# Optimization experiments

Hardware: AMD Instinct MI355X
Metric: run time of the kernel (lower is better)

## Reference

```python
import jax, jax.numpy as jnp
import numpy as np
import math

B = 256
IMG_H = IMG_W = 256
GH = GW = 64
HID = 512
NUM_GLIMPSES = 8


def _filterbank(delta_caps, center_caps, image_size, glimpse_size):
    # delta_caps, center_caps: (B,) in [-1, 1]
    I = float(image_size)
    G = float(glimpse_size)
    centers = (I - 1.0) * (center_caps + 1.0) / 2.0            # (B,)
    deltas = I / G * (1.0 - jnp.abs(delta_caps))               # (B,)
    gammas = jnp.exp(1.0 - 2.0 * jnp.abs(delta_caps))          # (B,)
    glimpse_pixels = jnp.arange(glimpse_size, dtype=jnp.float32) - (G - 1.0) / 2.0  # (G,)
    gp = centers[:, None] + deltas[:, None] * glimpse_pixels[None, :]               # (B, G)
    image_pixels = jnp.arange(image_size, dtype=jnp.float32)                        # (I,)
    fx = (image_pixels[None, None, :] - gp[:, :, None]) / gammas[:, None, None]     # (B, G, I)
    fx = 1.0 / (math.pi * gammas[:, None, None] * (1.0 + fx * fx))
    fx = fx / (jnp.sum(fx, axis=2, keepdims=True) + 1e-4)
    return jnp.transpose(fx, (0, 2, 1))  # (B, I, G)


def setup_inputs() -> dict:
    key = jax.random.key(0)
    ks = jax.random.split(key, 7)
    in_dim = GH * GW  # channels=1 (images come in as (B, h, w))
    return {
        "image_pairs": jax.random.normal(ks[0], (B, 2, IMG_H, IMG_W), dtype=jnp.float32),
        "W_ih": jax.random.normal(ks[1], (4 * HID, in_dim), dtype=jnp.float32) * 0.02,
        "W_hh": jax.random.normal(ks[2], (4 * HID, HID), dtype=jnp.float32) * 0.02,
        "b_ih": jax.random.normal(ks[3], (4 * HID,), dtype=jnp.float32) * 0.02,
        "b_hh": jax.random.normal(ks[4], (4 * HID,), dtype=jnp.float32) * 0.02,
        "W_g": jax.random.normal(ks[5], (3, HID), dtype=jnp.float32) * 0.02,
        "b_g": jax.random.normal(ks[6], (3,), dtype=jnp.float32) * 0.02,
    }


def _arc_forward(image_pairs, W_ih, W_hh, b_ih, b_hh, W_g, b_g):
    batch = image_pairs.shape[0]
    img0 = image_pairs[:, 0].astype(jnp.float32)  # (B, H, W)
    img1 = image_pairs[:, 1].astype(jnp.float32)

    def step(carry, t):
        Hx, Cx = carry
        images = jnp.where(t == 0, img0, img1)  # turn parity selects image
        gp = jnp.tanh(Hx @ W_g.T + b_g)         # (B, 3): (h_center, w_center, delta)
        F_h = _filterbank(gp[:, 2], gp[:, 0], IMG_H, GH)  # (B, H, GH)
        F_w = _filterbank(gp[:, 2], gp[:, 1], IMG_W, GW)  # (B, W, GW)
        # F_h^T @ images @ F_w  -> (B, GH, GW)
        g = jnp.einsum('bhg,bhw->bgw', F_h, images)
        g = jnp.einsum('bgw,bwj->bgj', g, F_w)
        x = g.reshape(batch, -1)  # (B, GH*GW)
        gates = x @ W_ih.T + b_ih + Hx @ W_hh.T + b_hh  # (B, 4*HID)
        i, f, gg, o = jnp.split(gates, 4, axis=1)       # torch LSTMCell gate order
        Cx = jax.nn.sigmoid(f) * Cx + jax.nn.sigmoid(i) * jnp.tanh(gg)
        Hx = jax.nn.sigmoid(o) * jnp.tanh(Cx)
        return (Hx, Cx), Hx

    init = (jnp.zeros((batch, HID), jnp.float32), jnp.zeros((batch, HID), jnp.float32))
    turns = jnp.arange(2 * NUM_GLIMPSES) % 2
    (Hx, Cx), all_hidden = jax.lax.scan(step, init, turns)
    return all_hidden[-1]  # (B, HID), last hidden state


def reference(image_pairs, W_ih, W_hh, b_ih, b_hh, W_g, b_g):
    return _arc_forward(image_pairs, W_ih, W_hh, b_ih, b_hh, W_g, b_g)
```

## Files before the change

kernel.cpp:

```cpp
#include <hip/hip_runtime.h>
#include <math.h>

#define NB 256
#define IMG 256
#define GSZ 64
#define HID 512
#define NSTEP 16
#define KTOT 4608
#define SPLITK 8
#define KCHUNK 576
#define KSTEPS 18

#define GP 264
#define SP 40
#define GLDS_BYTES (4*64*GP*2 + 512)

typedef unsigned short u16;
typedef __attribute__((ext_vector_type(8))) short s16x8;
typedef __attribute__((ext_vector_type(4))) float f32x4;

__device__ inline u16 f2bf(float f) {
    unsigned u = __float_as_uint(f);
    unsigned r = u + 0x7fffu + ((u >> 16) & 1u);
    return (u16)(r >> 16);
}
__device__ inline float bf2f(u16 h) { return __uint_as_float((unsigned)h << 16); }

__global__ __launch_bounds__(256) void k_wsplit(const float* __restrict__ W_ih,
                                                const float* __restrict__ W_hh,
                                                u16* __restrict__ wc_hi,
                                                u16* __restrict__ wc_lo) {
    const int nchunk = 2048 * KTOT / 4;
    const int stride = gridDim.x * blockDim.x;
    for (int c = blockIdx.x * blockDim.x + threadIdx.x; c < nchunk; c += stride) {
        const int j = c / (KTOT / 4);
        const int k = (c - j * (KTOT / 4)) * 4;
        float4 v;
        if (k < 4096) v = *(const float4*)&W_ih[(size_t)j * 4096 + k];
        else          v = *(const float4*)&W_hh[(size_t)j * 512 + (k - 4096)];
        float f[4] = {v.x, v.y, v.z, v.w};
        u16 hi[4], lo[4];
        #pragma unroll
        for (int i = 0; i < 4; ++i) {
            hi[i] = f2bf(f[i]);
            lo[i] = f2bf(f[i] - bf2f(hi[i]));
        }
        const size_t o = (size_t)j * KTOT + k;
        *(ushort4*)&wc_hi[o] = make_ushort4(hi[0], hi[1], hi[2], hi[3]);
        *(ushort4*)&wc_lo[o] = make_ushort4(lo[0], lo[1], lo[2], lo[3]);
    }
}

__global__ __launch_bounds__(64) void k_params(const float* __restrict__ Hx,
                                               const float* __restrict__ W_g,
                                               const float* __restrict__ b_g,
                                               float* __restrict__ params) {
    const int b = blockIdx.x;
    const int l = threadIdx.x;
    float s0 = 0.f, s1 = 0.f, s2 = 0.f;
    const float* h = Hx + (size_t)b * HID;
    for (int k = l; k < HID; k += 64) {
        float hv = h[k];
        s0 += hv * W_g[k];
        s1 += hv * W_g[HID + k];
        s2 += hv * W_g[2 * HID + k];
    }
    for (int off = 32; off; off >>= 1) {
        s0 += __shfl_xor(s0, off, 64);
        s1 += __shfl_xor(s1, off, 64);
        s2 += __shfl_xor(s2, off, 64);
    }
    if (l == 0) {
        float g0 = tanhf(s0 + b_g[0]);
        float g1 = tanhf(s1 + b_g[1]);
        float g2 = tanhf(s2 + b_g[2]);
        float ad = fabsf(g2);
        params[b * 4 + 0] = 127.5f * (g0 + 1.0f);
        params[b * 4 + 1] = 127.5f * (g1 + 1.0f);
        params[b * 4 + 2] = 4.0f * (1.0f - ad);
        params[b * 4 + 3] = expf(1.0f - 2.0f * ad);
    }
}

__global__ __launch_bounds__(256, 1) void k_glimpse(const float* __restrict__ params,
                                                    const float* __restrict__ imgs,
                                                    int sel,
                                                    u16* __restrict__ xh,
                                                    u16* __restrict__ xl) {
    extern __shared__ u16 sm[];
    u16* FwH  = sm;
    u16* FwL  = sm + 64 * GP;
    u16* R2   = sm + 2 * 64 * GP;
    u16* AstH = R2;
    u16* AstL = R2 + 256 * SP;
    u16* FhH  = R2;
    u16* FhL  = R2 + 64 * GP;
    float* invW = (float*)(sm + 4 * 64 * GP);
    float* invA = invW + 64;

    const int b = blockIdx.x, t = threadIdx.x;
    const int lane = t & 63, wv = t >> 6;
    const int fr = lane & 15, kg = lane >> 4;
    const float ch = params[b * 4 + 0];
    const float cw = params[b * 4 + 1];
    const float dl = params[b * 4 + 2];
    const float gm = params[b * 4 + 3];
    const float ig = 1.0f / gm;
    const float coef = 1.0f / (3.14159265358979323846f * gm);

    {
        const int r  = t >> 2;
        const int w0 = (t & 3) * 64;
        const float rc = cw + dl * ((float)r - 31.5f);
        float s = 0.f;
        for (int i = 0; i < 64; i += 4) {
            u16 hh[4], ll[4];
            #pragma unroll
            for (int j = 0; j < 4; ++j) {
                float u = ((float)(w0 + i + j) - rc) * ig;
                float val = coef / (1.0f + u * u);
                s += val;
                hh[j] = f2bf(val);
                ll[j] = f2bf(val - bf2f(hh[j]));
            }
            *(ushort4*)&FwH[r * GP + w0 + i] = make_ushort4(hh[0], hh[1], hh[2], hh[3]);
            *(ushort4*)&FwL[r * GP + w0 + i] = make_ushort4(ll[0], ll[1], ll[2], ll[3]);
        }
        s += __shfl_xor(s, 1, 64);
        s += __shfl_xor(s, 2, 64);
        if ((t & 3) == 0) invW[r] = 1.0f / (s + 1e-4f);
    }
    __syncthreads();

    const float* imgp = imgs + (size_t)(b * 2 + sel) * (IMG * IMG);
    int rowA[8], coA[8];
    float4 pf[8];
    #pragma unroll
    for (int q = 0; q < 8; ++q) {
        const int c = q * 256 + t;
        rowA[q] = c >> 3;
        coA[q]  = (c & 7) * 4;
        pf[q] = *(const float4*)&imgp[rowA[q] * IMG + coA[q]];
    }
    f32x4 acc[4][4];
    #pragma unroll
    for (int mi = 0; mi < 4; ++mi)
        #pragma unroll
        for (int ni = 0; ni < 4; ++ni) acc[mi][ni] = (f32x4)(0.f);

    for (int ks = 0; ks < 8; ++ks) {
        __syncthreads();
        #pragma unroll
        for (int q = 0; q < 8; ++q) {
            float f[4] = {pf[q].x, pf[q].y, pf[q].z, pf[q].w};
            u16 hh[4], ll[4];
            #pragma unroll
            for (int j = 0; j < 4; ++j) {
                hh[j] = f2bf(f[j]);
                ll[j] = f2bf(f[j] - bf2f(hh[j]));
            }
            *(ushort4*)&AstH[rowA[q] * SP + coA[q]] = make_ushort4(hh[0], hh[1], hh[2], hh[3]);
            *(ushort4*)&AstL[rowA[q] * SP + coA[q]] = make_ushort4(ll[0], ll[1], ll[2], ll[3]);
        }
        __syncthreads();
        if (ks < 7) {
            #pragma unroll
            for (int q = 0; q < 8; ++q)
                pf[q] = *(const float4*)&imgp[rowA[q] * IMG + (ks + 1) * 32 + coA[q]];
        }
        s16x8 ah[4], al[4], bh[4], bl[4];
        #pragma unroll
        for (int mi = 0; mi < 4; ++mi) {
            const int r = wv * 64 + mi * 16 + fr;
            ah[mi] = *(const s16x8*)&AstH[r * SP + kg * 8];
            al[mi] = *(const s16x8*)&AstL[r * SP + kg * 8];
        }
        #pragma unroll
        for (int ni = 0; ni < 4; ++ni) {
            const int r = ni * 16 + fr;
            bh[ni] = *(const s16x8*)&FwH[r * GP + ks * 32 + kg * 8];
            bl[ni] = *(const s16x8*)&FwL[r * GP + ks * 32 + kg * 8];
        }
        #pragma unroll
        for (int mi = 0; mi < 4; ++mi)
            #pragma unroll
            for (int ni = 0; ni < 4; ++ni) {
                acc[mi][ni] = __builtin_amdgcn_mfma_f32_16x16x32_bf16(ah[mi], bh[ni], acc[mi][ni], 0, 0, 0);
                acc[mi][ni] = __builtin_amdgcn_mfma_f32_16x16x32_bf16(ah[mi], bl[ni], acc[mi][ni], 0, 0, 0);
                acc[mi][ni] = __builtin_amdgcn_mfma_f32_16x16x32_bf16(al[mi], bh[ni], acc[mi][ni], 0, 0, 0);
            }
    }
    __syncthreads();

    #pragma unroll
    for (int ni = 0; ni < 4; ++ni) {
        const int col = ni * 16 + fr;
        const float s = invW[col];
        #pragma unroll
        for (int mi = 0; mi < 4; ++mi) {
            const int hbase = wv * 64 + mi * 16 + kg * 4;
            u16 hh[4], ll[4];
            #pragma unroll
            for (int r = 0; r < 4; ++r) {
                float v = acc[mi][ni][r] * s;
                hh[r] = f2bf(v);
                ll[r] = f2bf(v - bf2f(hh[r]));
            }
            *(ushort4*)&FwH[col * GP + hbase] = make_ushort4(hh[0], hh[1], hh[2], hh[3]);
            *(ushort4*)&FwL[col * GP + hbase] = make_ushort4(ll[0], ll[1], ll[2], ll[3]);
        }
    }

    {
        const int r  = t >> 2;
        const int h0 = (t & 3) * 64;
        const float rc = ch + dl * ((float)r - 31.5f);
        float s = 0.f;
        for (int i = 0; i < 64; i += 4) {
            u16 hh[4], ll[4];
            #pragma unroll
            for (int j = 0; j < 4; ++j) {
                float u = ((float)(h0 + i + j) - rc) * ig;
                float val = coef / (1.0f + u * u);
                s += val;
                hh[j] = f2bf(val);
                ll[j] = f2bf(val - bf2f(hh[j]));
            }
            *(ushort4*)&FhH[r * GP + h0 + i] = make_ushort4(hh[0], hh[1], hh[2], hh[3]);
            *(ushort4*)&FhL[r * GP + h0 + i] = make_ushort4(ll[0], ll[1], ll[2], ll[3]);
        }
        s += __shfl_xor(s, 1, 64);
        s += __shfl_xor(s, 2, 64);
        if ((t & 3) == 0) invA[r] = 1.0f / (s + 1e-4f);
    }
    __syncthreads();

    f32x4 acc2[4];
    #pragma unroll
    for (int ni = 0; ni < 4; ++ni) acc2[ni] = (f32x4)(0.f);

    #pragma unroll
    for (int ks = 0; ks < 8; ++ks) {
        const int ra = wv * 16 + fr;
        s16x8 a2h = *(const s16x8*)&FhH[ra * GP + ks * 32 + kg * 8];
        s16x8 a2l = *(const s16x8*)&FhL[ra * GP + ks * 32 + kg * 8];
        #pragma unroll
        for (int ni = 0; ni < 4; ++ni) {
            const int rb = ni * 16 + fr;
            s16x8 b2h = *(const s16x8*)&FwH[rb * GP + ks * 32 + kg * 8];
            s16x8 b2l = *(const s16x8*)&FwL[rb * GP + ks * 32 + kg * 8];
            acc2[ni] = __builtin_amdgcn_mfma_f32_16x16x32_bf16(a2h, b2h, acc2[ni], 0, 0, 0);
            acc2[ni] = __builtin_amdgcn_mfma_f32_16x16x32_bf16(a2h, b2l, acc2[ni], 0, 0, 0);
            acc2[ni] = __builtin_amdgcn_mfma_f32_16x16x32_bf16(a2l, b2h, acc2[ni], 0, 0, 0);
        }
    }
    const int rbase = wv * 16 + kg * 4;
    float ia[4];
    #pragma unroll
    for (int r = 0; r < 4; ++r) ia[r] = invA[rbase + r];
    u16* xho = xh + (size_t)b * KTOT;
    u16* xlo = xl + (size_t)b * KTOT;
    #pragma unroll
    for (int ni = 0; ni < 4; ++ni) {
        const int col = ni * 16 + fr;
        #pragma unroll
        for (int r = 0; r < 4; ++r) {
            float v = acc2[ni][r] * ia[r];
            u16 hv = f2bf(v);
            const int o = (rbase + r) * GSZ + col;
            xho[o] = hv;
            xlo[o] = f2bf(v - bf2f(hv));
        }
    }
}

__global__ __launch_bounds__(256) void k_gates(const u16* __restrict__ xcat_hi,
                                               const u16* __restrict__ xcat_lo,
                                               const u16* __restrict__ wc_hi,
                                               const u16* __restrict__ wc_lo,
                                               float* __restrict__ part) {
    __shared__ u16 smem[4][128][40];

    const int bid = blockIdx.x;
    const int mb = bid & 1;
    const int nb = (bid >> 1) & 15;
    const int kc = bid >> 5;
    const int m0 = mb * 128, n0 = nb * 128, k0 = kc * KCHUNK;
    const int t = threadIdx.x;
    const int lane = t & 63, wid = t >> 6;
    const int wm = wid >> 1, wn = wid & 1;
    const int fr = lane & 15, kg = lane >> 4;

    const u16* srcs[8];
    u16* dsts[8];
    #pragma unroll
    for (int q = 0; q < 8; ++q) {
        const int idx = ((q * 256 + t) & 511);
        const int row = idx >> 2;
        const int ko = (idx & 3) * 8;
        const int mat = q >> 1;
        const u16* gbase;
        if (mat == 0)      gbase = xcat_hi + (size_t)(m0 + row) * KTOT;
        else if (mat == 1) gbase = xcat_lo + (size_t)(m0 + row) * KTOT;
        else if (mat == 2) gbase = wc_hi + (size_t)(n0 + row) * KTOT;
        else               gbase = wc_lo + (size_t)(n0 + row) * KTOT;
        srcs[q] = gbase + k0 + ko;
        dsts[q] = &smem[mat][row][ko];
    }

    f32x4 acc[4][4];
    #pragma unroll
    for (int mi = 0; mi < 4; ++mi)
        #pragma unroll
        for (int ni = 0; ni < 4; ++ni) acc[mi][ni] = (f32x4)(0.f);

    s16x8 ld[8];
    #pragma unroll
    for (int q = 0; q < 8; ++q) ld[q] = *(const s16x8*)(srcs[q]);

    for (int ks = 0; ks < KSTEPS; ++ks) {
        __syncthreads();
        #pragma unroll
        for (int q = 0; q < 8; ++q) {
            *(s16x8*)(dsts[q]) = ld[q];
            srcs[q] += 32;
        }
        __syncthreads();
        if (ks + 1 < KSTEPS) {
            #pragma unroll
            for (int q = 0; q < 8; ++q) ld[q] = *(const s16x8*)(srcs[q]);
        }
        s16x8 ah[4], al[4], bh[4], bl[4];
        #pragma unroll
        for (int mi = 0; mi < 4; ++mi) {
            const int r = wm * 64 + mi * 16 + fr;
            ah[mi] = *(const s16x8*)&smem[0][r][kg * 8];
            al[mi] = *(const s16x8*)&smem[1][r][kg * 8];
        }
        #pragma unroll
        for (int ni = 0; ni < 4; ++ni) {
            const int r = wn * 64 + ni * 16 + fr;
            bh[ni] = *(const s16x8*)&smem[2][r][kg * 8];
            bl[ni] = *(const s16x8*)&smem[3][r][kg * 8];
        }
        #pragma unroll
        for (int mi = 0; mi < 4; ++mi)
            #pragma unroll
            for (int ni = 0; ni < 4; ++ni) {
                acc[mi][ni] = __builtin_amdgcn_mfma_f32_16x16x32_bf16(ah[mi], bh[ni], acc[mi][ni], 0, 0, 0);
                acc[mi][ni] = __builtin_amdgcn_mfma_f32_16x16x32_bf16(ah[mi], bl[ni], acc[mi][ni], 0, 0, 0);
                acc[mi][ni] = __builtin_amdgcn_mfma_f32_16x16x32_bf16(al[mi], bh[ni], acc[mi][ni], 0, 0, 0);
            }
    }

    float* pp = part + ((size_t)kc << 19);
    #pragma unroll
    for (int mi = 0; mi < 4; ++mi) {
        const int mbase = m0 + wm * 64 + mi * 16 + (lane >> 4) * 4;
        #pragma unroll
        for (int ni = 0; ni < 4; ++ni) {
            const int col = n0 + wn * 64 + ni * 16 + (lane & 15);
            #pragma unroll
            for (int r = 0; r < 4; ++r)
                pp[(size_t)(mbase + r) * 2048 + col] = acc[mi][ni][r];
        }
    }
}

__global__ __launch_bounds__(256) void k_lstm(const float* __restrict__ part,
                                              const float* __restrict__ b_ih,
                                              const float* __restrict__ b_hh,
                                              float* __restrict__ Cx,
                                              float* __restrict__ Hx,
                                              float* __restrict__ out,
                                              u16* __restrict__ xcat_hi,
                                              u16* __restrict__ xcat_lo) {
    const int id = blockIdx.x * 256 + threadIdx.x;
    const int b = id >> 9, u = id & (HID - 1);
    float gi = b_ih[u] + b_hh[u];
    float gf = b_ih[HID + u] + b_hh[HID + u];
    float gg = b_ih[2 * HID + u] + b_hh[2 * HID + u];
    float go = b_ih[3 * HID + u] + b_hh[3 * HID + u];
    const float* pb = part + (size_t)b * 2048;
    #pragma unroll
    for (int kc = 0; kc < SPLITK; ++kc) {
        const float* p = pb + (size_t)kc * (256 * 2048);
        gi += p[u];
        gf += p[HID + u];
        gg += p[2 * HID + u];
        go += p[3 * HID + u];
    }
    float si = 1.0f / (1.0f + expf(-gi));
    float sf = 1.0f / (1.0f + expf(-gf));
    float so = 1.0f / (1.0f + expf(-go));
    float c = sf * Cx[id] + si * tanhf(gg);
    float h = so * tanhf(c);
    Cx[id] = c;
    Hx[id] = h;
    out[id] = h;
    u16 hh = f2bf(h);
    xcat_hi[(size_t)b * KTOT + 4096 + u] = hh;
    xcat_lo[(size_t)b * KTOT + 4096 + u] = f2bf(h - bf2f(hh));
}

extern "C" void kernel_launch(void* const* d_in, const int* in_sizes, int n_in,
                              void* d_out, int out_size, void* d_ws, size_t ws_size,
                              hipStream_t stream) {
    const float* imgs = (const float*)d_in[0];
    const float* W_ih = (const float*)d_in[1];
    const float* W_hh = (const float*)d_in[2];
    const float* b_ih = (const float*)d_in[3];
    const float* b_hh = (const float*)d_in[4];
    const float* W_g  = (const float*)d_in[5];
    const float* b_g  = (const float*)d_in[6];
    float* out = (float*)d_out;

    char* w = (char*)d_ws;
    float* params  = (float*)w;  w += 4096;
    float* Hx      = (float*)w;  w += NB * HID * 4;
    float* Cx      = (float*)w;  w += NB * HID * 4;
    u16* xcat_hi   = (u16*)w;    w += (size_t)NB * KTOT * 2;
    u16* xcat_lo   = (u16*)w;    w += (size_t)NB * KTOT * 2;
    u16* wc_hi     = (u16*)w;    w += (size_t)2048 * KTOT * 2;
    u16* wc_lo     = (u16*)w;    w += (size_t)2048 * KTOT * 2;
    float* part    = (float*)w;  w += (size_t)SPLITK * NB * 2048 * 4;

    (void)hipFuncSetAttribute((const void*)k_glimpse,
                              hipFuncAttributeMaxDynamicSharedMemorySize, GLDS_BYTES);

    hipMemsetAsync(Hx, 0, (size_t)2 * NB * HID * sizeof(float), stream);
    hipMemsetAsync(xcat_hi, 0, (size_t)2 * NB * KTOT * 2, stream);

    k_wsplit<<<2304, 256, 0, stream>>>(W_ih, W_hh, wc_hi, wc_lo);

    for (int step = 0; step < NSTEP; ++step) {
        k_params<<<NB, 64, 0, stream>>>(Hx, W_g, b_g, params);
        k_glimpse<<<NB, 256, GLDS_BYTES, stream>>>(params, imgs, step & 1, xcat_hi, xcat_lo);
        k_gates<<<256, 256, 0, stream>>>(xcat_hi, xcat_lo, wc_hi, wc_lo, part);
        k_lstm<<<NB * HID / 256, 256, 0, stream>>>(part, b_ih, b_hh, Cx, Hx, out, xcat_hi, xcat_lo);
    }
}
```

Before: 1.020 ms.

## Fuse all LSTM glimpse steps into one persistent kernel with grid barriers

New measurement: 3.205 ms. 214% more time.

```diff
diff --git a/kernel.cpp b/kernel.cpp
--- a/kernel.cpp
+++ b/kernel.cpp
@@ -10,10 +10,8 @@
 #define SPLITK 8
 #define KCHUNK 576
 #define KSTEPS 18
-
-#define GP 264
 #define SP 40
-#define GLDS_BYTES (4*64*GP*2 + 512)
+#define TP 72
 
 typedef unsigned short u16;
 typedef __attribute__((ext_vector_type(8))) short s16x8;
@@ -25,382 +23,421 @@
     return (u16)(r >> 16);
 }
 __device__ inline float bf2f(u16 h) { return __uint_as_float((unsigned)h << 16); }
-
-__global__ __launch_bounds__(256) void k_wsplit(const float* __restrict__ W_ih,
-                                                const float* __restrict__ W_hh,
-                                                u16* __restrict__ wc_hi,
-                                                u16* __restrict__ wc_lo) {
-    const int nchunk = 2048 * KTOT / 4;
-    const int stride = gridDim.x * blockDim.x;
-    for (int c = blockIdx.x * blockDim.x + threadIdx.x; c < nchunk; c += stride) {
-        const int j = c / (KTOT / 4);
-        const int k = (c - j * (KTOT / 4)) * 4;
-        float4 v;
-        if (k < 4096) v = *(const float4*)&W_ih[(size_t)j * 4096 + k];
-        else          v = *(const float4*)&W_hh[(size_t)j * 512 + (k - 4096)];
-        float f[4] = {v.x, v.y, v.z, v.w};
-        u16 hi[4], lo[4];
-        #pragma unroll
-        for (int i = 0; i < 4; ++i) {
-            hi[i] = f2bf(f[i]);
-            lo[i] = f2bf(f[i] - bf2f(hi[i]));
-        }
-        const size_t o = (size_t)j * KTOT + k;
-        *(ushort4*)&wc_hi[o] = make_ushort4(hi[0], hi[1], hi[2], hi[3]);
-        *(ushort4*)&wc_lo[o] = make_ushort4(lo[0], lo[1], lo[2], lo[3]);
+__device__ inline float sigm(float v) { return 1.0f / (1.0f + expf(-v)); }
+
+__device__ inline void gridbar(int* bar, int gen) {
+    __threadfence();
+    __syncthreads();
+    const int b = blockIdx.x, t = threadIdx.x;
+    if (b == 0) {
+        if (t > 0) {
+            while (__hip_atomic_load(&bar[1 + t], __ATOMIC_ACQUIRE,
+                                     __HIP_MEMORY_SCOPE_AGENT) < gen)
+                __builtin_amdgcn_s_sleep(2);
+        }
+        __syncthreads();
+        if (t == 0)
+            __hip_atomic_store(&bar[0], gen, __ATOMIC_RELEASE,
+                               __HIP_MEMORY_SCOPE_AGENT);
+    } else {
+        if (t == 0) {
+            __hip_atomic_store(&bar[1 + b], gen, __ATOMIC_RELEASE,
+                               __HIP_MEMORY_SCOPE_AGENT);
+            while (__hip_atomic_load(&bar[0], __ATOMIC_ACQUIRE,
+                                     __HIP_MEMORY_SCOPE_AGENT) < gen)
+                __builtin_amdgcn_s_sleep(2);
+        }
+        __syncthreads();
     }
 }
 
-__global__ __launch_bounds__(64) void k_params(const float* __restrict__ Hx,
-                                               const float* __restrict__ W_g,
-                                               const float* __restrict__ b_g,
-                                               float* __restrict__ params) {
-    const int b = blockIdx.x;
-    const int l = threadIdx.x;
-    float s0 = 0.f, s1 = 0.f, s2 = 0.f;
-    const float* h = Hx + (size_t)b * HID;
-    for (int k = l; k < HID; k += 64) {
-        float hv = h[k];
-        s0 += hv * W_g[k];
-        s1 += hv * W_g[HID + k];
-        s2 += hv * W_g[2 * HID + k];
-    }
-    for (int off = 32; off; off >>= 1) {
-        s0 += __shfl_xor(s0, off, 64);
-        s1 += __shfl_xor(s1, off, 64);
-        s2 += __shfl_xor(s2, off, 64);
-    }
-    if (l == 0) {
-        float g0 = tanhf(s0 + b_g[0]);
-        float g1 = tanhf(s1 + b_g[1]);
-        float g2 = tanhf(s2 + b_g[2]);
-        float ad = fabsf(g2);
-        params[b * 4 + 0] = 127.5f * (g0 + 1.0f);
-        params[b * 4 + 1] = 127.5f * (g1 + 1.0f);
-        params[b * 4 + 2] = 4.0f * (1.0f - ad);
-        params[b * 4 + 3] = expf(1.0f - 2.0f * ad);
-    }
-}
-
-__global__ __launch_bounds__(256, 1) void k_glimpse(const float* __restrict__ params,
-                                                    const float* __restrict__ imgs,
-                                                    int sel,
-                                                    u16* __restrict__ xh,
-                                                    u16* __restrict__ xl) {
-    extern __shared__ u16 sm[];
-    u16* FwH  = sm;
-    u16* FwL  = sm + 64 * GP;
-    u16* R2   = sm + 2 * 64 * GP;
-    u16* AstH = R2;
-    u16* AstL = R2 + 256 * SP;
-    u16* FhH  = R2;
-    u16* FhL  = R2 + 64 * GP;
-    float* invW = (float*)(sm + 4 * 64 * GP);
-    float* invA = invW + 64;
+__global__ __launch_bounds__(256, 2) void k_all(
+    const float* __restrict__ imgs, const float* __restrict__ W_ih,
+    const float* __restrict__ W_hh, const float* __restrict__ b_ih,
+    const float* __restrict__ b_hh, const float* __restrict__ W_g,
+    const float* __restrict__ b_g,
+    int* __restrict__ bar,
+    u16* __restrict__ wc_hi, u16* __restrict__ wc_lo,
+    u16* __restrict__ xcat_hi, u16* __restrict__ xcat_lo,
+    float* __restrict__ part, float* __restrict__ out)
+{
+    __shared__ __align__(16) u16 sm[25600];
+    __shared__ float invW[64];
+    __shared__ float invA[64];
+    __shared__ float red[12];
+    u16* AstH = sm;
+    u16* AstL = sm + 10240;
+    u16* FwcH = sm + 20480;
+    u16* FwcL = sm + 23040;
+    u16* t1TH = sm;
+    u16* t1TL = sm + 4608;
+    u16* FhcH = sm + 9216;
+    u16* FhcL = sm + 13824;
+    u16 (*gsm)[128][40] = (u16 (*)[128][40])sm;
 
     const int b = blockIdx.x, t = threadIdx.x;
     const int lane = t & 63, wv = t >> 6;
     const int fr = lane & 15, kg = lane >> 4;
-    const float ch = params[b * 4 + 0];
-    const float cw = params[b * 4 + 1];
-    const float dl = params[b * 4 + 2];
-    const float gm = params[b * 4 + 3];
-    const float ig = 1.0f / gm;
-    const float coef = 1.0f / (3.14159265358979323846f * gm);
+
+    float hx0 = 0.f, hx1 = 0.f, cx0 = 0.f, cx1 = 0.f;
 
     {
-        const int r  = t >> 2;
-        const int w0 = (t & 3) * 64;
-        const float rc = cw + dl * ((float)r - 31.5f);
-        float s = 0.f;
-        for (int i = 0; i < 64; i += 4) {
-            u16 hh[4], ll[4];
-            #pragma unroll
-            for (int j = 0; j < 4; ++j) {
-                float u = ((float)(w0 + i + j) - rc) * ig;
-                float val = coef / (1.0f + u * u);
-                s += val;
-                hh[j] = f2bf(val);
-                ll[j] = f2bf(val - bf2f(hh[j]));
-            }
-            *(ushort4*)&FwH[r * GP + w0 + i] = make_ushort4(hh[0], hh[1], hh[2], hh[3]);
-            *(ushort4*)&FwL[r * GP + w0 + i] = make_ushort4(ll[0], ll[1], ll[2], ll[3]);
-        }
-        s += __shfl_xor(s, 1, 64);
-        s += __shfl_xor(s, 2, 64);
-        if ((t & 3) == 0) invW[r] = 1.0f / (s + 1e-4f);
+        const int nchunk = 2048 * KTOT / 4;
+        for (int c = b * 256 + t; c < nchunk; c += 65536) {
+            const int j = c / (KTOT / 4);
+            const int k = (c - j * (KTOT / 4)) * 4;
+            float4 v;
+            if (k < 4096) v = *(const float4*)&W_ih[(size_t)j * 4096 + k];
+            else          v = *(const float4*)&W_hh[(size_t)j * 512 + (k - 4096)];
+            float f[4] = {v.x, v.y, v.z, v.w};
+            u16 hi[4], lo[4];
+            #pragma unroll
+            for (int i = 0; i < 4; ++i) {
+                hi[i] = f2bf(f[i]);
+                lo[i] = f2bf(f[i] - bf2f(hi[i]));
+            }
+            const size_t o = (size_t)j * KTOT + k;
+            *(ushort4*)&wc_hi[o] = make_ushort4(hi[0], hi[1], hi[2], hi[3]);
+            *(ushort4*)&wc_lo[o] = make_ushort4(lo[0], lo[1], lo[2], lo[3]);
+        }
     }
-    __syncthreads();
-
-    const float* imgp = imgs + (size_t)(b * 2 + sel) * (IMG * IMG);
-    int rowA[8], coA[8];
-    float4 pf[8];
-    #pragma unroll
-    for (int q = 0; q < 8; ++q) {
-        const int c = q * 256 + t;
-        rowA[q] = c >> 3;
-        coA[q]  = (c & 7) * 4;
-        pf[q] = *(const float4*)&imgp[rowA[q] * IMG + coA[q]];
-    }
-    f32x4 acc[4][4];
-    #pragma unroll
-    for (int mi = 0; mi < 4; ++mi)
-        #pragma unroll
-        for (int ni = 0; ni < 4; ++ni) acc[mi][ni] = (f32x4)(0.f);
-
-    for (int ks = 0; ks < 8; ++ks) {
-        __syncthreads();
+
+    for (int step = 0; step < NSTEP; ++step) {
+        if (step == 0) {
+            const size_t o = (size_t)b * KTOT + 4096 + t;
+            xcat_hi[o] = 0;       xcat_lo[o] = 0;
+            xcat_hi[o + 256] = 0; xcat_lo[o + 256] = 0;
+        } else {
+            #pragma unroll
+            for (int half = 0; half < 2; ++half) {
+                const int u = t + half * 256;
+                float gi = b_ih[u] + b_hh[u];
+                float gf = b_ih[HID + u] + b_hh[HID + u];
+                float gg = b_ih[2 * HID + u] + b_hh[2 * HID + u];
+                float go = b_ih[3 * HID + u] + b_hh[3 * HID + u];
+                const float* pb = part + (size_t)b * 2048;
+                #pragma unroll
+                for (int kc = 0; kc < SPLITK; ++kc) {
+                    const float* p = pb + (size_t)kc * (256 * 2048);
+                    gi += p[u];
+                    gf += p[HID + u];
+                    gg += p[2 * HID + u];
+                    go += p[3 * HID + u];
+                }
+                float co = half ? cx1 : cx0;
+                float c = sigm(gf) * co + sigm(gi) * tanhf(gg);
+                float h = sigm(go) * tanhf(c);
+                if (half) { cx1 = c; hx1 = h; } else { cx0 = c; hx0 = h; }
+                u16 hh = f2bf(h);
+                xcat_hi[(size_t)b * KTOT + 4096 + u] = hh;
+                xcat_lo[(size_t)b * KTOT + 4096 + u] = f2bf(h - bf2f(hh));
+            }
+        }
+        float s0 = hx0 * W_g[t] + hx1 * W_g[t + 256];
+        float s1 = hx0 * W_g[HID + t] + hx1 * W_g[HID + t + 256];
+        float s2 = hx0 * W_g[2 * HID + t] + hx1 * W_g[2 * HID + t + 256];
+        for (int off = 32; off; off >>= 1) {
+            s0 += __shfl_xor(s0, off, 64);
+            s1 += __shfl_xor(s1, off, 64);
+            s2 += __shfl_xor(s2, off, 64);
+        }
+        __syncthreads();
+        if (lane == 0) { red[wv * 3 + 0] = s0; red[wv * 3 + 1] = s1; red[wv * 3 + 2] = s2; }
+        __syncthreads();
+        s0 = red[0] + red[3] + red[6] + red[9];
+        s1 = red[1] + red[4] + red[7] + red[10];
+        s2 = red[2] + red[5] + red[8] + red[11];
+        const float g0 = tanhf(s0 + b_g[0]);
+        const float g1 = tanhf(s1 + b_g[1]);
+        const float g2 = tanhf(s2 + b_g[2]);
+        const float ad = fabsf(g2);
+        const float ch = 127.5f * (g0 + 1.0f);
+        const float cw = 127.5f * (g1 + 1.0f);
+        const float dl = 4.0f * (1.0f - ad);
+        const float gm = expf(1.0f - 2.0f * ad);
+        const float ig = 1.0f / gm;
+        const float coef = 1.0f / (3.14159265358979323846f * gm);
+
+        const int fwr = t >> 2;
+        const int fwc = (t & 3) * 8;
+        const float rcw = cw + dl * ((float)fwr - 31.5f);
+        float rsW = 0.f;
+
+        const float* imgp = imgs + (size_t)(b * 2 + (step & 1)) * (IMG * IMG);
+        int rowA[8], coA[8];
+        float4 pf[8];
         #pragma unroll
         for (int q = 0; q < 8; ++q) {
-            float f[4] = {pf[q].x, pf[q].y, pf[q].z, pf[q].w};
-            u16 hh[4], ll[4];
-            #pragma unroll
-            for (int j = 0; j < 4; ++j) {
-                hh[j] = f2bf(f[j]);
-                ll[j] = f2bf(f[j] - bf2f(hh[j]));
-            }
-            *(ushort4*)&AstH[rowA[q] * SP + coA[q]] = make_ushort4(hh[0], hh[1], hh[2], hh[3]);
-            *(ushort4*)&AstL[rowA[q] * SP + coA[q]] = make_ushort4(ll[0], ll[1], ll[2], ll[3]);
-        }
-        __syncthreads();
-        if (ks < 7) {
-            #pragma unroll
-            for (int q = 0; q < 8; ++q)
-                pf[q] = *(const float4*)&imgp[rowA[q] * IMG + (ks + 1) * 32 + coA[q]];
-        }
-        s16x8 ah[4], al[4], bh[4], bl[4];
+            const int c = q * 256 + t;
+            rowA[q] = c >> 3;
+            coA[q]  = (c & 7) * 4;
+            pf[q] = *(const float4*)&imgp[rowA[q] * IMG + coA[q]];
+        }
+        f32x4 acc[4][4];
+        #pragma unroll
+        for (int mi = 0; mi < 4; ++mi)
+            #pragma unroll
+            for (int ni = 0; ni < 4; ++ni) acc[mi][ni] = (f32x4)(0.f);
+
+        for (int ks = 0; ks < 8; ++ks) {
+            __syncthreads();
+            #pragma unroll
+            for (int q = 0; q < 8; ++q) {
+                float f[4] = {pf[q].x, pf[q].y, pf[q].z, pf[q].w};
+                u16 hh[4], ll[4];
+                #pragma unroll
+                for (int j = 0; j < 4; ++j) {
+                    hh[j] = f2bf(f[j]);
+                    ll[j] = f2bf(f[j] - bf2f(hh[j]));
+                }
+                *(ushort4*)&AstH[rowA[q] * SP + coA[q]] = make_ushort4(hh[0], hh[1], hh[2], hh[3]);
+                *(ushort4*)&AstL[rowA[q] * SP + coA[q]] = make_ushort4(ll[0], ll[1], ll[2], ll[3]);
+            }
+            {
+                u16 hh[8], ll[8];
+                #pragma unroll
+                for (int j = 0; j < 8; ++j) {
+                    float u = ((float)(ks * 32 + fwc + j) - rcw) * ig;
+                    float val = coef / (1.0f + u * u);
+                    rsW += val;
+                    hh[j] = f2bf(val);
+                    ll[j] = f2bf(val - bf2f(hh[j]));
+                }
+                *(ushort4*)&FwcH[fwr * SP + fwc]     = make_ushort4(hh[0], hh[1], hh[2], hh[3]);
+                *(ushort4*)&FwcH[fwr * SP + fwc + 4] = make_ushort4(hh[4], hh[5], hh[6], hh[7]);
+                *(ushort4*)&FwcL[fwr * SP + fwc]     = make_ushort4(ll[0], ll[1], ll[2], ll[3]);
+                *(ushort4*)&FwcL[fwr * SP + fwc + 4] = make_ushort4(ll[4], ll[5], ll[6], ll[7]);
+            }
+            __syncthreads();
+            if (ks < 7) {
+                #pragma unroll
+                for (int q = 0; q < 8; ++q)
+                    pf[q] = *(const float4*)&imgp[rowA[q] * IMG + (ks + 1) * 32 + coA[q]];
+            }
+            s16x8 ah[4], al[4], bh[4], bl[4];
+            #pragma unroll
+            for (int mi = 0; mi < 4; ++mi) {
+                const int r = mi * 16 + fr;
+                ah[mi] = *(const s16x8*)&FwcH[r * SP + kg * 8];
+                al[mi] = *(const s16x8*)&FwcL[r * SP + kg * 8];
+            }
+            #pragma unroll
+            for (int ni = 0; ni < 4; ++ni) {
+                const int r = wv * 64 + ni * 16 + fr;
+                bh[ni] = *(const s16x8*)&AstH[r * SP + kg * 8];
+                bl[ni] = *(const s16x8*)&AstL[r * SP + kg * 8];
+            }
+            #pragma unroll
+            for (int mi = 0; mi < 4; ++mi)
+                #pragma unroll
+                for (int ni = 0; ni < 4; ++ni) {
+                    acc[mi][ni] = __builtin_amdgcn_mfma_f32_16x16x32_bf16(ah[mi], bh[ni], acc[mi][ni], 0, 0, 0);
+                    acc[mi][ni] = __builtin_amdgcn_mfma_f32_16x16x32_bf16(ah[mi], bl[ni], acc[mi][ni], 0, 0, 0);
+                    acc[mi][ni] = __builtin_amdgcn_mfma_f32_16x16x32_bf16(al[mi], bh[ni], acc[mi][ni], 0, 0, 0);
+                }
+        }
+        rsW += __shfl_xor(rsW, 1, 64);
+        rsW += __shfl_xor(rsW, 2, 64);
+        if ((t & 3) == 0) invW[fwr] = 1.0f / (rsW + 1e-4f);
+        __syncthreads();
         #pragma unroll
         for (int mi = 0; mi < 4; ++mi) {
-            const int r = wv * 64 + mi * 16 + fr;
-            ah[mi] = *(const s16x8*)&AstH[r * SP + kg * 8];
-            al[mi] = *(const s16x8*)&AstL[r * SP + kg * 8];
-        }
+            float w4[4];
+            #pragma unroll
+            for (int r = 0; r < 4; ++r) w4[r] = invW[mi * 16 + kg * 4 + r];
+            #pragma unroll
+            for (int ni = 0; ni < 4; ++ni)
+                #pragma unroll
+                for (int r = 0; r < 4; ++r) acc[mi][ni][r] *= w4[r];
+        }
+
+        f32x4 xacc[4];
         #pragma unroll
-        for (int ni = 0; ni < 4; ++ni) {
-            const int r = ni * 16 + fr;
-            bh[ni] = *(const s16x8*)&FwH[r * GP + ks * 32 + kg * 8];
-            bl[ni] = *(const s16x8*)&FwL[r * GP + ks * 32 + kg * 8];
-        }
+        for (int ni = 0; ni < 4; ++ni) xacc[ni] = (f32x4)(0.f);
+        const int fhr = t >> 2;
+        const int fhc = (t & 3) * 16;
+        const float rch = ch + dl * ((float)fhr - 31.5f);
+        float rsA = 0.f;
+
+        for (int p = 0; p < 4; ++p) {
+            __syncthreads();
+            #pragma unroll
+            for (int blk = 0; blk < 4; ++blk) {
+                u16 hh[4], ll[4];
+                #pragma unroll
+                for (int j = 0; j < 4; ++j) {
+                    float u = ((float)(p * 64 + fhc + blk * 4 + j) - rch) * ig;
+                    float val = coef / (1.0f + u * u);
+                    rsA += val;
+                    hh[j] = f2bf(val);
+                    ll[j] = f2bf(val - bf2f(hh[j]));
+                }
+                *(ushort4*)&FhcH[fhr * TP + fhc + blk * 4] = make_ushort4(hh[0], hh[1], hh[2], hh[3]);
+                *(ushort4*)&FhcL[fhr * TP + fhc + blk * 4] = make_ushort4(ll[0], ll[1], ll[2], ll[3]);
+            }
+            if (wv == p) {
+                #pragma unroll
+                for (int mi = 0; mi < 4; ++mi)
+                    #pragma unroll
+                    for (int ni = 0; ni < 4; ++ni)
+                        #pragma unroll
+                        for (int r = 0; r < 4; ++r) {
+                            const int row = mi * 16 + kg * 4 + r;
+                            const int col = ni * 16 + fr;
+                            float v = acc[mi][ni][r];
+                            u16 hv = f2bf(v);
+                            t1TH[row * TP + col] = hv;
+                            t1TL[row * TP + col] = f2bf(v - bf2f(hv));
+                        }
+            }
+            __syncthreads();
+            #pragma unroll
+            for (int k2 = 0; k2 < 2; ++k2) {
+                const int ra = wv * 16 + fr;
+                s16x8 a2h = *(const s16x8*)&FhcH[ra * TP + k2 * 32 + kg * 8];
+                s16x8 a2l = *(const s16x8*)&FhcL[ra * TP + k2 * 32 + kg * 8];
+                #pragma unroll
+                for (int ni = 0; ni < 4; ++ni) {
+                    const int rb = ni * 16 + fr;
+                    s16x8 b2h = *(const s16x8*)&t1TH[rb * TP + k2 * 32 + kg * 8];
+                    s16x8 b2l = *(const s16x8*)&t1TL[rb * TP + k2 * 32 + kg * 8];
+                    xacc[ni] = __builtin_amdgcn_mfma_f32_16x16x32_bf16(a2h, b2h, xacc[ni], 0, 0, 0);
+                    xacc[ni] = __builtin_amdgcn_mfma_f32_16x16x32_bf16(a2h, b2l, xacc[ni], 0, 0, 0);
+                    xacc[ni] = __builtin_amdgcn_mfma_f32_16x16x32_bf16(a2l, b2h, xacc[ni], 0, 0, 0);
+                }
+            }
+        }
+        rsA += __shfl_xor(rsA, 1, 64);
+        rsA += __shfl_xor(rsA, 2, 64);
+        if ((t & 3) == 0) invA[fhr] = 1.0f / (rsA + 1e-4f);
+        __syncthreads();
+        {
+            float ia[4];
+            #pragma unroll
+            for (int r = 0; r < 4; ++r) ia[r] = invA[wv * 16 + kg * 4 + r];
+            u16* xho = xcat_hi + (size_t)b * KTOT;
+            u16* xlo = xcat_lo + (size_t)b * KTOT;
+            #pragma unroll
+            for (int ni = 0; ni < 4; ++ni) {
+                const int col = ni * 16 + fr;
+                #pragma unroll
+                for (int r = 0; r < 4; ++r) {
+                    float v = xacc[ni][r] * ia[r];
+                    u16 hv = f2bf(v);
+                    const int o = (wv * 16 + kg * 4 + r) * GSZ + col;
+                    xho[o] = hv;
+                    xlo[o] = f2bf(v - bf2f(hv));
+                }
+            }
+        }
+        gridbar(bar, 2 * step + 1);
+
+        {
+            const int mb = b & 1;
+            const int nb = (b >> 1) & 15;
+            const int kc = b >> 5;
+            const int m0 = mb * 128, n0 = nb * 128, k0 = kc * KCHUNK;
+            const int wm = wv >> 1, wn = wv & 1;
+
+            const u16* srcs[8];
+            u16* dsts[8];
+            #pragma unroll
+            for (int q = 0; q < 8; ++q) {
+                const int idx = ((q * 256 + t) & 511);
+                const int row = idx >> 2;
+                const int ko = (idx & 3) * 8;
+                const int mat = q >> 1;
+                const u16* gbase;
+                if (mat == 0)      gbase = xcat_hi + (size_t)(m0 + row) * KTOT;
+                else if (mat == 1) gbase = xcat_lo + (size_t)(m0 + row) * KTOT;
+                else if (mat == 2) gbase = wc_hi + (size_t)(n0 + row) * KTOT;
+                else               gbase = wc_lo + (size_t)(n0 + row) * KTOT;
+                srcs[q] = gbase + k0 + ko;
+                dsts[q] = &gsm[mat][row][ko];
+            }
+
+            f32x4 gacc[4][4];
+            #pragma unroll
+            for (int mi = 0; mi < 4; ++mi)
+                #pragma unroll
+                for (int ni = 0; ni < 4; ++ni) gacc[mi][ni] = (f32x4)(0.f);
+
+            s16x8 ld[8];
+            #pragma unroll
+            for (int q = 0; q < 8; ++q) ld[q] = *(const s16x8*)(srcs[q]);
+
+            for (int ks = 0; ks < KSTEPS; ++ks) {
+                __syncthreads();
+                #pragma unroll
+                for (int q = 0; q < 8; ++q) {
+                    *(s16x8*)(dsts[q]) = ld[q];
+                    srcs[q] += 32;
+                }
+                __syncthreads();
+                if (ks + 1 < KSTEPS) {
+                    #pragma unroll
+                    for (int q = 0; q < 8; ++q) ld[q] = *(const s16x8*)(srcs[q]);
+                }
+                s16x8 ah[4], al[4], bh[4], bl[4];
+                #pragma unroll
+                for (int mi = 0; mi < 4; ++mi) {
+                    const int r = wm * 64 + mi * 16 + fr;
+                    ah[mi] = *(const s16x8*)&gsm[0][r][kg * 8];
+                    al[mi] = *(const s16x8*)&gsm[1][r][kg * 8];
+                }
+                #pragma unroll
+                for (int ni = 0; ni < 4; ++ni) {
+                    const int r = wn * 64 + ni * 16 + fr;
+                    bh[ni] = *(const s16x8*)&gsm[2][r][kg * 8];
+                    bl[ni] = *(const s16x8*)&gsm[3][r][kg * 8];
+                }
+                #pragma unroll
+                for (int mi = 0; mi < 4; ++mi)
+                    #pragma unroll
+                    for (int ni = 0; ni < 4; ++ni) {
+                        gacc[mi][ni] = __builtin_amdgcn_mfma_f32_16x16x32_bf16(ah[mi], bh[ni], gacc[mi][ni], 0, 0, 0);
+                        gacc[mi][ni] = __builtin_amdgcn_mfma_f32_16x16x32_bf16(ah[mi], bl[ni], gacc[mi][ni], 0, 0, 0);
+                        gacc[mi][ni] = __builtin_amdgcn_mfma_f32_16x16x32_bf16(al[mi], bh[ni], gacc[mi][ni], 0, 0, 0);
+                    }
+            }
+
+            float* pp = part + ((size_t)kc << 19);
+            #pragma unroll
+            for (int mi = 0; mi < 4; ++mi) {
+                const int mbase = m0 + wm * 64 + mi * 16 + kg * 4;
+                #pragma unroll
+                for (int ni = 0; ni < 4; ++ni) {
+                    const int col = n0 + wn * 64 + ni * 16 + fr;
+                    #pragma unroll
+                    for (int r = 0; r < 4; ++r)
+                        pp[(size_t)(mbase + r) * 2048 + col] = gacc[mi][ni][r];
+                }
+            }
+        }
+        gridbar(bar, 2 * step + 2);
+    }
+
+    #pragma unroll
+    for (int half = 0; half < 2; ++half) {
+        const int u = t + half * 256;
+        float gi = b_ih[u] + b_hh[u];
+        float gf = b_ih[HID + u] + b_hh[HID + u];
+        float gg = b_ih[2 * HID + u] + b_hh[2 * HID + u];
+        float go = b_ih[3 * HID + u] + b_hh[3 * HID + u];
+        const float* pb = part + (size_t)b * 2048;
         #pragma unroll
-        for (int mi = 0; mi < 4; ++mi)
-            #pragma unroll
-            for (int ni = 0; ni < 4; ++ni) {
-                acc[mi][ni] = __builtin_amdgcn_mfma_f32_16x16x32_bf16(ah[mi], bh[ni], acc[mi][ni], 0, 0, 0);
-                acc[mi][ni] = __builtin_amdgcn_mfma_f32_16x16x32_bf16(ah[mi], bl[ni], acc[mi][ni], 0, 0, 0);
-                acc[mi][ni] = __builtin_amdgcn_mfma_f32_16x16x32_bf16(al[mi], bh[ni], acc[mi][ni], 0, 0, 0);
-            }
+        for (int kc = 0; kc < SPLITK; ++kc) {
+            const float* p = pb + (size_t)kc * (256 * 2048);
+            gi += p[u];
+            gf += p[HID + u];
+            gg += p[2 * HID + u];
+            go += p[3 * HID + u];
+        }
+        float co = half ? cx1 : cx0;
+        float c = sigm(gf) * co + sigm(gi) * tanhf(gg);
+        float h = sigm(go) * tanhf(c);
+        out[(size_t)b * HID + u] = h;
     }
-    __syncthreads();
-
-    #pragma unroll
-    for (int ni = 0; ni < 4; ++ni) {
-        const int col = ni * 16 + fr;
-        const float s = invW[col];
-        #pragma unroll
-        for (int mi = 0; mi < 4; ++mi) {
-            const int hbase = wv * 64 + mi * 16 + kg * 4;
-            u16 hh[4], ll[4];
-            #pragma unroll
-            for (int r = 0; r < 4; ++r) {
-                float v = acc[mi][ni][r] * s;
-                hh[r] = f2bf(v);
-                ll[r] = f2bf(v - bf2f(hh[r]));
-            }
-            *(ushort4*)&FwH[col * GP + hbase] = make_ushort4(hh[0], hh[1], hh[2], hh[3]);
-            *(ushort4*)&FwL[col * GP + hbase] = make_ushort4(ll[0], ll[1], ll[2], ll[3]);
-        }
-    }
-
-    {
-        const int r  = t >> 2;
-        const int h0 = (t & 3) * 64;
-        const float rc = ch + dl * ((float)r - 31.5f);
-        float s = 0.f;
-        for (int i = 0; i < 64; i += 4) {
-            u16 hh[4], ll[4];
-            #pragma unroll
-            for (int j = 0; j < 4; ++j) {
-                float u = ((float)(h0 + i + j) - rc) * ig;
-                float val = coef / (1.0f + u * u);
-                s += val;
-                hh[j] = f2bf(val);
-                ll[j] = f2bf(val - bf2f(hh[j]));
-            }
-            *(ushort4*)&FhH[r * GP + h0 + i] = make_ushort4(hh[0], hh[1], hh[2], hh[3]);
-            *(ushort4*)&FhL[r * GP + h0 + i] = make_ushort4(ll[0], ll[1], ll[2], ll[3]);
-        }
-        s += __shfl_xor(s, 1, 64);
-        s += __shfl_xor(s, 2, 64);
-        if ((t & 3) == 0) invA[r] = 1.0f / (s + 1e-4f);
-    }
-    __syncthreads();
-
-    f32x4 acc2[4];
-    #pragma unroll
-    for (int ni = 0; ni < 4; ++ni) acc2[ni] = (f32x4)(0.f);
-
-    #pragma unroll
-    for (int ks = 0; ks < 8; ++ks) {
-        const int ra = wv * 16 + fr;
-        s16x8 a2h = *(const s16x8*)&FhH[ra * GP + ks * 32 + kg * 8];
-        s16x8 a2l = *(const s16x8*)&FhL[ra * GP + ks * 32 + kg * 8];
-        #pragma unroll
-        for (int ni = 0; ni < 4; ++ni) {
-            const int rb = ni * 16 + fr;
-            s16x8 b2h = *(const s16x8*)&FwH[rb * GP + ks * 32 + kg * 8];
-            s16x8 b2l = *(const s16x8*)&FwL[rb * GP + ks * 32 + kg * 8];
-            acc2[ni] = __builtin_amdgcn_mfma_f32_16x16x32_bf16(a2h, b2h, acc2[ni], 0, 0, 0);
-            acc2[ni] = __builtin_amdgcn_mfma_f32_16x16x32_bf16(a2h, b2l, acc2[ni], 0, 0, 0);
-            acc2[ni] = __builtin_amdgcn_mfma_f32_16x16x32_bf16(a2l, b2h, acc2[ni], 0, 0, 0);
-        }
-    }
-    const int rbase = wv * 16 + kg * 4;
-    float ia[4];
-    #pragma unroll
-    for (int r = 0; r < 4; ++r) ia[r] = invA[rbase + r];
-    u16* xho = xh + (size_t)b * KTOT;
-    u16* xlo = xl + (size_t)b * KTOT;
-    #pragma unroll
-    for (int ni = 0; ni < 4; ++ni) {
-        const int col = ni * 16 + fr;
-        #pragma unroll
-        for (int r = 0; r < 4; ++r) {
-            float v = acc2[ni][r] * ia[r];
-            u16 hv = f2bf(v);
-            const int o = (rbase + r) * GSZ + col;
-            xho[o] = hv;
-            xlo[o] = f2bf(v - bf2f(hv));
-        }
-    }
-}
-
-__global__ __launch_bounds__(256) void k_gates(const u16* __restrict__ xcat_hi,
-                                               const u16* __restrict__ xcat_lo,
-                                               const u16* __restrict__ wc_hi,
-                                               const u16* __restrict__ wc_lo,
-                                               float* __restrict__ part) {
-    __shared__ u16 smem[4][128][40];
-
-    const int bid = blockIdx.x;
-    const int mb = bid & 1;
-    const int nb = (bid >> 1) & 15;
-    const int kc = bid >> 5;
-    const int m0 = mb * 128, n0 = nb * 128, k0 = kc * KCHUNK;
-    const int t = threadIdx.x;
-    const int lane = t & 63, wid = t >> 6;
-    const int wm = wid >> 1, wn = wid & 1;
-    const int fr = lane & 15, kg = lane >> 4;
-
-    const u16* srcs[8];
-    u16* dsts[8];
-    #pragma unroll
-    for (int q = 0; q < 8; ++q) {
-        const int idx = ((q * 256 + t) & 511);
-        const int row = idx >> 2;
-        const int ko = (idx & 3) * 8;
-        const int mat = q >> 1;
-        const u16* gbase;
-        if (mat == 0)      gbase = xcat_hi + (size_t)(m0 + row) * KTOT;
-        else if (mat == 1) gbase = xcat_lo + (size_t)(m0 + row) * KTOT;
-        else if (mat == 2) gbase = wc_hi + (size_t)(n0 + row) * KTOT;
-        else               gbase = wc_lo + (size_t)(n0 + row) * KTOT;
-        srcs[q] = gbase + k0 + ko;
-        dsts[q] = &smem[mat][row][ko];
-    }
-
-    f32x4 acc[4][4];
-    #pragma unroll
-    for (int mi = 0; mi < 4; ++mi)
-        #pragma unroll
-        for (int ni = 0; ni < 4; ++ni) acc[mi][ni] = (f32x4)(0.f);
-
-    s16x8 ld[8];
-    #pragma unroll
-    for (int q = 0; q < 8; ++q) ld[q] = *(const s16x8*)(srcs[q]);
-
-    for (int ks = 0; ks < KSTEPS; ++ks) {
-        __syncthreads();
-        #pragma unroll
-        for (int q = 0; q < 8; ++q) {
-            *(s16x8*)(dsts[q]) = ld[q];
-            srcs[q] += 32;
-        }
-        __syncthreads();
-        if (ks + 1 < KSTEPS) {
-            #pragma unroll
-            for (int q = 0; q < 8; ++q) ld[q] = *(const s16x8*)(srcs[q]);
-        }
-        s16x8 ah[4], al[4], bh[4], bl[4];
-        #pragma unroll
-        for (int mi = 0; mi < 4; ++mi) {
-            const int r = wm * 64 + mi * 16 + fr;
-            ah[mi] = *(const s16x8*)&smem[0][r][kg * 8];
-            al[mi] = *(const s16x8*)&smem[1][r][kg * 8];
-        }
-        #pragma unroll
-        for (int ni = 0; ni < 4; ++ni) {
-            const int r = wn * 64 + ni * 16 + fr;
-            bh[ni] = *(const s16x8*)&smem[2][r][kg * 8];
-            bl[ni] = *(const s16x8*)&smem[3][r][kg * 8];
-        }
-        #pragma unroll
-        for (int mi = 0; mi < 4; ++mi)
-            #pragma unroll
-            for (int ni = 0; ni < 4; ++ni) {
-                acc[mi][ni] = __builtin_amdgcn_mfma_f32_16x16x32_bf16(ah[mi], bh[ni], acc[mi][ni], 0, 0, 0);
-                acc[mi][ni] = __builtin_amdgcn_mfma_f32_16x16x32_bf16(ah[mi], bl[ni], acc[mi][ni], 0, 0, 0);
-                acc[mi][ni] = __builtin_amdgcn_mfma_f32_16x16x32_bf16(al[mi], bh[ni], acc[mi][ni], 0, 0, 0);
-            }
-    }
-
-    float* pp = part + ((size_t)kc << 19);
-    #pragma unroll
-    for (int mi = 0; mi < 4; ++mi) {
-        const int mbase = m0 + wm * 64 + mi * 16 + (lane >> 4) * 4;
-        #pragma unroll
-        for (int ni = 0; ni < 4; ++ni) {
-            const int col = n0 + wn * 64 + ni * 16 + (lane & 15);
-            #pragma unroll
-            for (int r = 0; r < 4; ++r)
-                pp[(size_t)(mbase + r) * 2048 + col] = acc[mi][ni][r];
-        }
-    }
-}
-
-__global__ __launch_bounds__(256) void k_lstm(const float* __restrict__ part,
-                                              const float* __restrict__ b_ih,
-                                              const float* __restrict__ b_hh,
-                                              float* __restrict__ Cx,
-                                              float* __restrict__ Hx,
-                                              float* __restrict__ out,
-                                              u16* __restrict__ xcat_hi,
-                                              u16* __restrict__ xcat_lo) {
-    const int id = blockIdx.x * 256 + threadIdx.x;
-    const int b = id >> 9, u = id & (HID - 1);
-    float gi = b_ih[u] + b_hh[u];
-    float gf = b_ih[HID + u] + b_hh[HID + u];
-    float gg = b_ih[2 * HID + u] + b_hh[2 * HID + u];
-    float go = b_ih[3 * HID + u] + b_hh[3 * HID + u];
-    const float* pb = part + (size_t)b * 2048;
-    #pragma unroll
-    for (int kc = 0; kc < SPLITK; ++kc) {
-        const float* p = pb + (size_t)kc * (256 * 2048);
-        gi += p[u];
-        gf += p[HID + u];
-        gg += p[2 * HID + u];
-        go += p[3 * HID + u];
-    }
-    float si = 1.0f / (1.0f + expf(-gi));
-    float sf = 1.0f / (1.0f + expf(-gf));
-    float so = 1.0f / (1.0f + expf(-go));
-    float c = sf * Cx[id] + si * tanhf(gg);
-    float h = so * tanhf(c);
-    Cx[id] = c;
-    Hx[id] = h;
-    out[id] = h;
-    u16 hh = f2bf(h);
-    xcat_hi[(size_t)b * KTOT + 4096 + u] = hh;
-    xcat_lo[(size_t)b * KTOT + 4096 + u] = f2bf(h - bf2f(hh));
 }
 
 extern "C" void kernel_launch(void* const* d_in, const int* in_sizes, int n_in,
@@ -416,27 +453,15 @@
     float* out = (float*)d_out;
 
     char* w = (char*)d_ws;
-    float* params  = (float*)w;  w += 4096;
-    float* Hx      = (float*)w;  w += NB * HID * 4;
-    float* Cx      = (float*)w;  w += NB * HID * 4;
+    int* bar       = (int*)w;    w += 4096;
     u16* xcat_hi   = (u16*)w;    w += (size_t)NB * KTOT * 2;
     u16* xcat_lo   = (u16*)w;    w += (size_t)NB * KTOT * 2;
     u16* wc_hi     = (u16*)w;    w += (size_t)2048 * KTOT * 2;
     u16* wc_lo     = (u16*)w;    w += (size_t)2048 * KTOT * 2;
     float* part    = (float*)w;  w += (size_t)SPLITK * NB * 2048 * 4;
 
-    (void)hipFuncSetAttribute((const void*)k_glimpse,
-                              hipFuncAttributeMaxDynamicSharedMemorySize, GLDS_BYTES);
-
-    hipMemsetAsync(Hx, 0, (size_t)2 * NB * HID * sizeof(float), stream);
-    hipMemsetAsync(xcat_hi, 0, (size_t)2 * NB * KTOT * 2, stream);
-
-    k_wsplit<<<2304, 256, 0, stream>>>(W_ih, W_hh, wc_hi, wc_lo);
-
-    for (int step = 0; step < NSTEP; ++step) {
-        k_params<<<NB, 64, 0, stream>>>(Hx, W_g, b_g, params);
-        k_glimpse<<<NB, 256, GLDS_BYTES, stream>>>(params, imgs, step & 1, xcat_hi, xcat_lo);
-        k_gates<<<256, 256, 0, stream>>>(xcat_hi, xcat_lo, wc_hi, wc_lo, part);
-        k_lstm<<<NB * HID / 256, 256, 0, stream>>>(part, b_ih, b_hh, Cx, Hx, out, xcat_hi, xcat_lo);
-    }
+    hipMemsetAsync(bar, 0, 4096, stream);
+
+    k_all<<<NB, 256, 0, stream>>>(imgs, W_ih, W_hh, b_ih, b_hh, W_g, b_g,
+                                  bar, wc_hi, wc_lo, xcat_hi, xcat_lo, part, out);
 }
```
